# Optimization experiments

Measured on AMD Instinct MI355X. Metric: run time of the kernel, lower is better.

Reference implementation:

```python
import jax, jax.numpy as jnp
import numpy as np

T, N, DH, E = 4, 50000, 64, 800000
BN_EPS = 1e-5


def setup_inputs() -> dict:
    key = jax.random.key(0)
    ks = jax.random.split(key, 8)
    node_data = jax.random.normal(ks[0], (T, N, DH), dtype=jnp.float32)
    edge_weight = jax.random.uniform(ks[1], (E,), dtype=jnp.float32)
    W1 = jax.random.normal(ks[2], (DH, 3 * DH), dtype=jnp.float32) * 0.05
    b1 = jax.random.normal(ks[3], (DH,), dtype=jnp.float32) * 0.05
    gamma = jnp.ones((3 * DH,), dtype=jnp.float32)
    beta = jnp.zeros((3 * DH,), dtype=jnp.float32)
    src = jax.random.randint(ks[4], (E,), 0, N)
    dst = jax.random.randint(ks[5], (E,), 0, N)
    return {"node_data": node_data, "edge_weight": edge_weight, "W1": W1,
            "b1": b1, "gamma": gamma, "beta": beta, "src": src, "dst": dst}


def reference(node_data, edge_weight, W1, b1, gamma, beta, src, dst):
    # --- sparse weighted neighbor aggregation (torch.bmm with sparse ew) ---
    # msg[t, e, :] = w_e * x[t, src_e, :]
    msg = node_data[:, src, :] * edge_weight[None, :, None]          # [T, E, dh]
    agg = jnp.zeros((T, N, DH), jnp.float32).at[:, dst, :].add(msg)  # [T, N, dh]
    # Z = torch.sparse.sum(ew, dim=2); Z[Z==0]=1 (degree normalization)
    Z = jnp.zeros((N,), jnp.float32).at[dst].add(edge_weight)
    Z = jnp.where(Z == 0, 1.0, Z)
    avg_neighbor = agg / Z[None, :, None]
    # prev_state: zeros at t=0, shifted node_data otherwise
    prev = jnp.concatenate([jnp.zeros((1, N, DH), jnp.float32), node_data[:-1]], axis=0)
    inp = jnp.concatenate([node_data, prev, avg_neighbor], axis=2).reshape(T * N, 3 * DH)
    # --- ReluFCN with batchnorm (training-mode batch stats, biased var) ---
    mu = jnp.mean(inp, axis=0)
    var = jnp.mean(jnp.square(inp - mu), axis=0)
    xhat = (inp - mu) * jax.lax.rsqrt(var + BN_EPS) * gamma + beta
    out = jax.nn.relu(xhat @ W1.T + b1)
    return out.reshape(T, N, DH)
```

## Files before the change

### kernel.cpp

```cpp
#include <hip/hip_runtime.h>

#define TT 4
#define NN 50000
#define DH 64
#define EE 800000
#define BN_EPS 1e-5f
#define NB 196
#define G1 64
#define G2 256
#define EB 2048
#define AGG_B 2048
#define AGG_W (AGG_B*4)
#define MAIN_B 2048
#define FOLD_B 8

typedef __attribute__((ext_vector_type(8))) short short8;
typedef __attribute__((ext_vector_type(4))) float floatx4;

#define WS_DEG      0
#define WS_FLAGS    200704
#define WS_ROWSTART 201728
#define WS_PX       401920
#define WS_PX2      467456
#define WS_PA       532992
#define WS_PA2      598528
#define WS_W1EFF    664064
#define WS_B1EFF    688640
#define WS_PACKED   1048576
#define WS_XB       8388608
#define WS_AVGB     34078720
#define WS_RANK     34078720

__device__ __forceinline__ unsigned short f2b(float f) {
    unsigned int u = __float_as_uint(f);
    unsigned int r = (u + 0x7FFFu + ((u >> 16) & 1u)) >> 16;
    return (unsigned short)r;
}
__device__ __forceinline__ float b2f(unsigned short u) {
    return __uint_as_float((unsigned int)u << 16);
}

__global__ __launch_bounds__(256) void k_prep_stats(
    const float* __restrict__ x, unsigned short* __restrict__ xb,
    float* __restrict__ PX, float* __restrict__ PX2,
    int* __restrict__ deg, int* __restrict__ flags) {
    int t = blockIdx.y;
    int tid = threadIdx.x;
    int pb = t * G1 + blockIdx.x;
    int gid = pb * 256 + tid;
    if (gid < NN) deg[gid] = 0;
    else if (gid < NN + NB) flags[gid - NN] = 0;

    int g = blockIdx.x * 256 + tid;
    const floatx4* xt = (const floatx4*)(x + (size_t)t * NN * 64);
    float s[4] = {0.f, 0.f, 0.f, 0.f}, s2[4] = {0.f, 0.f, 0.f, 0.f};
    for (int v = g; v < NN * 16; v += G1 * 256) {
        floatx4 d = __builtin_nontemporal_load(&xt[v]);
        ushort4 o;
        o.x = f2b(d.x); o.y = f2b(d.y); o.z = f2b(d.z); o.w = f2b(d.w);
        *(ushort4*)(xb + (size_t)(v >> 4) * 256 + t * 64 + (v & 15) * 4) = o;
        s[0] += d.x; s2[0] += d.x * d.x;
        s[1] += d.y; s2[1] += d.y * d.y;
        s[2] += d.z; s2[2] += d.z * d.z;
        s[3] += d.w; s2[3] += d.w * d.w;
    }
    __shared__ float ls[256 * 4], ls2[256 * 4];
#pragma unroll
    for (int j = 0; j < 4; ++j) { ls[tid * 4 + j] = s[j]; ls2[tid * 4 + j] = s2[j]; }
    __syncthreads();
    if (tid < 64) {
        int g16 = tid >> 2, comp = tid & 3;
        float rs = 0.f, rs2 = 0.f;
#pragma unroll
        for (int k = 0; k < 16; ++k) {
            int j = g16 + 16 * k;
            rs += ls[j * 4 + comp]; rs2 += ls2[j * 4 + comp];
        }
        int slot = (t * G1 + blockIdx.x) * 64 + tid;
        PX[slot] = rs; PX2[slot] = rs2;
    }
}

__global__ __launch_bounds__(256) void k_rank(const int* __restrict__ dst,
                                              int* __restrict__ deg,
                                              int* __restrict__ rank) {
    for (int e = blockIdx.x * 256 + threadIdx.x; e < EE; e += EB * 256)
        rank[e] = atomicAdd(&deg[dst[e]], 1);
}

__global__ __launch_bounds__(256) void k_scan_lb(
    const int* __restrict__ deg, int* __restrict__ flags,
    int* __restrict__ row_start) {
    int b = blockIdx.x, tid = threadIdx.x;
    int i = b * 256 + tid;
    int v = (i < NN) ? deg[i] : 0;
    __shared__ int ls[256];
    ls[tid] = v;
    __syncthreads();
    for (int off = 1; off < 256; off <<= 1) {
        int t = (tid >= off) ? ls[tid - off] : 0;
        __syncthreads();
        ls[tid] += t;
        __syncthreads();
    }
    int incl = ls[tid];
    if (tid == 0) atomicExch(&flags[b], ls[255] + 1);
    __shared__ int pre_s;
    if (tid == 0) pre_s = 0;
    __syncthreads();
    if (tid < b) {
        int f;
        do { f = atomicAdd(&flags[tid], 0); } while (f == 0);
        atomicAdd(&pre_s, f - 1);
    }
    __syncthreads();
    int excl = pre_s + incl - v;
    if (i < NN) row_start[i] = excl;
    if (i == NN - 1) row_start[NN] = excl + v;
}

__global__ __launch_bounds__(256) void k_fill2(
    const int* __restrict__ src, const int* __restrict__ dst,
    const float* __restrict__ ew, const int* __restrict__ rank,
    const int* __restrict__ row_start, int2* __restrict__ packed) {
    for (int e = blockIdx.x * 256 + threadIdx.x; e < EE; e += EB * 256) {
        int p = row_start[dst[e]] + rank[e];
        packed[p] = make_int2(src[e], __float_as_int(ew[e]));
    }
}

__global__ __launch_bounds__(256) void k_agg(
    const unsigned short* __restrict__ xb, const int2* __restrict__ packed,
    const int* __restrict__ row_start, unsigned short* __restrict__ avgb) {
    int wv = __builtin_amdgcn_readfirstlane(threadIdx.x >> 6);
    int l = threadIdx.x & 63;
    int wgid = blockIdx.x * 4 + wv;
    const ushort4* xl = (const ushort4*)xb + l;
    for (int n = wgid; n < NN; n += AGG_W) {
        int rs = row_start[n], re = row_start[n + 1];
        float a0 = 0.f, a1 = 0.f, a2 = 0.f, a3 = 0.f, wsum = 0.f;
        for (int e = rs; e < re; e += 8) {
            int rem = re - e;
            int2 p[8];
#pragma unroll
            for (int j = 0; j < 8; ++j) p[j] = packed[e + j];
            ushort4 v[8];
#pragma unroll
            for (int j = 0; j < 8; ++j) {
                int sidx = (j < rem) ? p[j].x : 0;
                v[j] = xl[(size_t)sidx * 64];
            }
#pragma unroll
            for (int j = 0; j < 8; ++j) {
                float w = (j < rem) ? __int_as_float(p[j].y) : 0.f;
                wsum += w;
                a0 = fmaf(w, b2f(v[j].x), a0);
                a1 = fmaf(w, b2f(v[j].y), a1);
                a2 = fmaf(w, b2f(v[j].z), a2);
                a3 = fmaf(w, b2f(v[j].w), a3);
            }
        }
        float rz = (wsum == 0.f) ? 1.f : (1.f / wsum);
        ushort4 o;
        o.x = f2b(a0 * rz); o.y = f2b(a1 * rz);
        o.z = f2b(a2 * rz); o.w = f2b(a3 * rz);
        *((ushort4*)avgb + (size_t)n * 64 + l) = o;
    }
}

__global__ __launch_bounds__(256) void k_stats_avg(
    const unsigned short* __restrict__ avgb, float* __restrict__ PA,
    float* __restrict__ PA2) {
    int tid = threadIdx.x;
    int g = blockIdx.x * 256 + tid;
    const short8* av = (const short8*)avgb;
    float s[8], s2[8];
#pragma unroll
    for (int j = 0; j < 8; ++j) { s[j] = 0.f; s2[j] = 0.f; }
    for (int v = g; v < TT * NN * 8; v += G2 * 256) {
        short8 d = av[v];
#pragma unroll
        for (int j = 0; j < 8; ++j) {
            float f = b2f((unsigned short)d[j]);
            s[j] += f; s2[j] += f * f;
        }
    }
    __shared__ float ls[256 * 8], ls2[256 * 8];
#pragma unroll
    for (int j = 0; j < 8; ++j) { ls[tid * 8 + j] = s[j]; ls2[tid * 8 + j] = s2[j]; }
    __syncthreads();
    if (tid < 64) {
        int g8 = tid >> 3, comp = tid & 7;
        float rs = 0.f, rs2 = 0.f;
#pragma unroll
        for (int k = 0; k < 32; ++k) {
            int j = g8 + 8 * k;
            rs += ls[j * 8 + comp]; rs2 += ls2[j * 8 + comp];
        }
        PA[blockIdx.x * 64 + tid] = rs;
        PA2[blockIdx.x * 64 + tid] = rs2;
    }
}

__global__ void k_fold(const float* __restrict__ W1, const float* __restrict__ b1,
                       const float* __restrict__ gamma, const float* __restrict__ beta,
                       const float* __restrict__ PX, const float* __restrict__ PX2,
                       const float* __restrict__ PA, const float* __restrict__ PA2,
                       unsigned short* __restrict__ W1eff, float* __restrict__ b1eff) {
    __shared__ float gS[192], hS[192];
    int c = threadIdx.x;
    const float inv = 1.0f / (float)(TT * NN);
    if (c < 192) {
        float s = 0.f, s2 = 0.f;
        if (c < 64) {
            for (int i = 0; i < TT * G1; ++i) { s += PX[i * 64 + c]; s2 += PX2[i * 64 + c]; }
        } else if (c < 128) {
            int cc = c - 64;
            for (int i = 0; i < (TT - 1) * G1; ++i) { s += PX[i * 64 + cc]; s2 += PX2[i * 64 + cc]; }
        } else {
            int cc = c - 128;
            for (int i = 0; i < G2; ++i) { s += PA[i * 64 + cc]; s2 += PA2[i * 64 + cc]; }
        }
        float mu = s * inv, ex2 = s2 * inv;
        float var = ex2 - mu * mu;
        float g = gamma[c] / sqrtf(var + BN_EPS);
        gS[c] = g;
        hS[c] = beta[c] - mu * g;
    }
    __syncthreads();
    for (int i = blockIdx.x * 192 + c; i < 64 * 192; i += FOLD_B * 192)
        W1eff[i] = f2b(W1[i] * gS[c]);
    if (c < 8) {
        int o = blockIdx.x * 8 + c;
        float acc = b1[o];
        for (int cc = 0; cc < 192; ++cc) acc += hS[cc] * W1[o * 192 + cc];
        b1eff[o] = acc;
    }
}

__global__ __launch_bounds__(256) void k_main(
    const unsigned short* __restrict__ xb, const unsigned short* __restrict__ avgb,
    const unsigned short* __restrict__ Wb, const float* __restrict__ bias,
    float* __restrict__ out) {
    int wave = threadIdx.x >> 6;
    int lane = threadIdx.x & 63;
    int m = lane & 15;
    int q = lane >> 4;
    const short8 zf = (short8){0, 0, 0, 0, 0, 0, 0, 0};

    for (int tile = blockIdx.x; tile < (TT * NN) / 64; tile += MAIN_B) {
        int r0 = tile * 64 + wave * 16;
        int t = r0 / NN;
        int n0 = r0 - t * NN;

        size_t nb = (size_t)(n0 + m) * 256 + (size_t)t * 64 + q * 8;
        const unsigned short* xrow = xb + nb;
        const unsigned short* arow = avgb + nb;
        bool has_prev = (t >= 1);

        floatx4 acc[4];
#pragma unroll
        for (int ct = 0; ct < 4; ++ct) acc[ct] = (floatx4){0.f, 0.f, 0.f, 0.f};

#pragma unroll
        for (int kc = 0; kc < 6; ++kc) {
            short8 a;
            if (kc < 2) {
                a = *(const short8*)(xrow + kc * 32);
            } else if (kc < 4) {
                a = has_prev ? *(const short8*)(xrow - 64 + (kc - 2) * 32) : zf;
            } else {
                a = *(const short8*)(arow + (kc - 4) * 32);
            }
#pragma unroll
            for (int ct = 0; ct < 4; ++ct) {
                short8 b = *(const short8*)(Wb + (size_t)(ct * 16 + m) * 192 + kc * 32 + q * 8);
                acc[ct] = __builtin_amdgcn_mfma_f32_16x16x32_bf16(a, b, acc[ct], 0, 0, 0);
            }
        }

#pragma unroll
        for (int ct = 0; ct < 4; ++ct) {
            float bv = bias[ct * 16 + m];
#pragma unroll
            for (int i = 0; i < 4; ++i) {
                int row = q * 4 + i;
                __builtin_nontemporal_store(fmaxf(acc[ct][i] + bv, 0.f),
                                            &out[(size_t)(r0 + row) * 64 + ct * 16 + m]);
            }
        }
    }
}

extern "C" void kernel_launch(void* const* d_in, const int* in_sizes, int n_in,
                              void* d_out, int out_size, void* d_ws, size_t ws_size,
                              hipStream_t stream) {
    const float* x     = (const float*)d_in[0];
    const float* ew    = (const float*)d_in[1];
    const float* W1    = (const float*)d_in[2];
    const float* b1    = (const float*)d_in[3];
    const float* gamma = (const float*)d_in[4];
    const float* beta  = (const float*)d_in[5];
    const int*   src   = (const int*)d_in[6];
    const int*   dst   = (const int*)d_in[7];
    float* out = (float*)d_out;
    char*  ws  = (char*)d_ws;

    int*   deg      = (int*)(ws + WS_DEG);
    int*   flags    = (int*)(ws + WS_FLAGS);
    int*   row_start= (int*)(ws + WS_ROWSTART);
    float* PX       = (float*)(ws + WS_PX);
    float* PX2      = (float*)(ws + WS_PX2);
    float* PA       = (float*)(ws + WS_PA);
    float* PA2      = (float*)(ws + WS_PA2);
    unsigned short* W1eff = (unsigned short*)(ws + WS_W1EFF);
    float* b1eff    = (float*)(ws + WS_B1EFF);
    int2*  packed   = (int2*)(ws + WS_PACKED);
    unsigned short* xb   = (unsigned short*)(ws + WS_XB);
    unsigned short* avgb = (unsigned short*)(ws + WS_AVGB);
    int*   rank     = (int*)(ws + WS_RANK);

    k_prep_stats<<<dim3(G1, TT), 256, 0, stream>>>(x, xb, PX, PX2, deg, flags);

    k_rank<<<EB, 256, 0, stream>>>(dst, deg, rank);

    k_scan_lb<<<NB, 256, 0, stream>>>(deg, flags, row_start);

    k_fill2<<<EB, 256, 0, stream>>>(src, dst, ew, rank, row_start, packed);

    k_agg<<<AGG_B, 256, 0, stream>>>(xb, packed, row_start, avgb);

    k_stats_avg<<<G2, 256, 0, stream>>>(avgb, PA, PA2);

    k_fold<<<FOLD_B, 192, 0, stream>>>(W1, b1, gamma, beta, PX, PX2, PA, PA2, W1eff, b1eff);

    k_main<<<MAIN_B, 256, 0, stream>>>(xb, avgb, W1eff, b1eff, out);
}
```

Before: 316.1 us.

## Fuse CSR build into cooperative kernel with sharded degree counters; fuse avg stats into agg

Replaces the separate rank, scan and fill kernels with one cooperative kernel that keeps dst and rank in registers across grid syncs. Degree atomics are spread over 8 shards to cut contention. The per-column statistics of the averaged neighbours are now accumulated inside the aggregation kernel, which removes a second pass over avgb. The cost is four grid-wide barriers, a dependence on cooperative launch residency (1024 blocks), and a fold step that now reduces 2048 partial sums instead of 256.

```diff
diff --git a/kernel.cpp b/kernel.cpp
--- a/kernel.cpp
+++ b/kernel.cpp
@@ -1,14 +1,19 @@
 #include <hip/hip_runtime.h>
+#include <hip/hip_cooperative_groups.h>
+
+namespace cg = cooperative_groups;
 
 #define TT 4
 #define NN 50000
 #define DH 64
 #define EE 800000
 #define BN_EPS 1e-5f
-#define NB 196
 #define G1 64
-#define G2 256
-#define EB 2048
+#define NSH 8
+#define NBLD 1024
+#define BTH (NBLD*256)
+#define EPT 4
+#define NBSC 196
 #define AGG_B 2048
 #define AGG_W (AGG_B*4)
 #define MAIN_B 2048
@@ -18,18 +23,17 @@
 typedef __attribute__((ext_vector_type(4))) float floatx4;
 
 #define WS_DEG      0
-#define WS_FLAGS    200704
-#define WS_ROWSTART 201728
-#define WS_PX       401920
-#define WS_PX2      467456
-#define WS_PA       532992
-#define WS_PA2      598528
-#define WS_W1EFF    664064
-#define WS_B1EFF    688640
-#define WS_PACKED   1048576
-#define WS_XB       8388608
-#define WS_AVGB     34078720
-#define WS_RANK     34078720
+#define WS_PA       0
+#define WS_PA2      524288
+#define WS_PART     1600000
+#define WS_ROWSTART 1601024
+#define WS_PX       1801088
+#define WS_PX2      1866624
+#define WS_W1EFF    1932160
+#define WS_B1EFF    1956736
+#define WS_PACKED   1957376
+#define WS_XB       8357888
+#define WS_AVGB     33957888
 
 __device__ __forceinline__ unsigned short f2b(float f) {
     unsigned int u = __float_as_uint(f);
@@ -43,13 +47,11 @@
 __global__ __launch_bounds__(256) void k_prep_stats(
     const float* __restrict__ x, unsigned short* __restrict__ xb,
     float* __restrict__ PX, float* __restrict__ PX2,
-    int* __restrict__ deg, int* __restrict__ flags) {
+    int* __restrict__ deg) {
     int t = blockIdx.y;
     int tid = threadIdx.x;
-    int pb = t * G1 + blockIdx.x;
-    int gid = pb * 256 + tid;
-    if (gid < NN) deg[gid] = 0;
-    else if (gid < NN + NB) flags[gid - NN] = 0;
+    int zid = (t * G1 + blockIdx.x) * 256 + tid;
+    for (int i = zid; i < NSH * NN; i += 65536) deg[i] = 0;
 
     int g = blockIdx.x * 256 + tid;
     const floatx4* xt = (const floatx4*)(x + (size_t)t * NN * 64);
@@ -81,61 +83,99 @@
     }
 }
 
-__global__ __launch_bounds__(256) void k_rank(const int* __restrict__ dst,
-                                              int* __restrict__ deg,
-                                              int* __restrict__ rank) {
-    for (int e = blockIdx.x * 256 + threadIdx.x; e < EE; e += EB * 256)
-        rank[e] = atomicAdd(&deg[dst[e]], 1);
-}
-
-__global__ __launch_bounds__(256) void k_scan_lb(
-    const int* __restrict__ deg, int* __restrict__ flags,
-    int* __restrict__ row_start) {
-    int b = blockIdx.x, tid = threadIdx.x;
-    int i = b * 256 + tid;
-    int v = (i < NN) ? deg[i] : 0;
+__global__ __launch_bounds__(256, 4) void k_build(
+    const int* __restrict__ src, const int* __restrict__ dst,
+    const float* __restrict__ ew,
+    int* __restrict__ deg,
+    int* __restrict__ part,
+    int* __restrict__ row_start,
+    int2* __restrict__ packed) {
+    cg::grid_group grid = cg::this_grid();
+    int tid = threadIdx.x, bid = blockIdx.x;
+    int gtid = bid * 256 + tid;
+    int sh = bid & (NSH - 1);
+
+    int dstR[EPT], rnkR[EPT];
+#pragma unroll
+    for (int k = 0; k < EPT; ++k) {
+        int e = gtid + k * BTH;
+        if (e < EE) {
+            int d = dst[e];
+            dstR[k] = d;
+            rnkR[k] = atomicAdd(&deg[sh * NN + d], 1);
+        }
+    }
+    grid.sync();
+
     __shared__ int ls[256];
-    ls[tid] = v;
+    __shared__ int lsp[256];
+    int n = gtid;
+    int tot = 0;
+    if (n < NN) {
+        int run = 0;
+#pragma unroll
+        for (int s = 0; s < NSH; ++s) {
+            int c = deg[s * NN + n];
+            deg[s * NN + n] = run;
+            run += c;
+        }
+        tot = run;
+    }
+    ls[tid] = tot;
     __syncthreads();
     for (int off = 1; off < 256; off <<= 1) {
-        int t = (tid >= off) ? ls[tid - off] : 0;
+        int tv = (tid >= off) ? ls[tid - off] : 0;
         __syncthreads();
-        ls[tid] += t;
+        ls[tid] += tv;
         __syncthreads();
     }
     int incl = ls[tid];
-    if (tid == 0) atomicExch(&flags[b], ls[255] + 1);
-    __shared__ int pre_s;
-    if (tid == 0) pre_s = 0;
-    __syncthreads();
-    if (tid < b) {
-        int f;
-        do { f = atomicAdd(&flags[tid], 0); } while (f == 0);
-        atomicAdd(&pre_s, f - 1);
-    }
-    __syncthreads();
-    int excl = pre_s + incl - v;
-    if (i < NN) row_start[i] = excl;
-    if (i == NN - 1) row_start[NN] = excl + v;
-}
-
-__global__ __launch_bounds__(256) void k_fill2(
-    const int* __restrict__ src, const int* __restrict__ dst,
-    const float* __restrict__ ew, const int* __restrict__ rank,
-    const int* __restrict__ row_start, int2* __restrict__ packed) {
-    for (int e = blockIdx.x * 256 + threadIdx.x; e < EE; e += EB * 256) {
-        int p = row_start[dst[e]] + rank[e];
-        packed[p] = make_int2(src[e], __float_as_int(ew[e]));
+    if (tid == 255 && bid < NBSC) part[bid] = incl;
+    grid.sync();
+
+    if (bid == 0) {
+        int v = (tid < NBSC) ? part[tid] : 0;
+        lsp[tid] = v;
+        __syncthreads();
+        for (int off = 1; off < 256; off <<= 1) {
+            int tv = (tid >= off) ? lsp[tid - off] : 0;
+            __syncthreads();
+            lsp[tid] += tv;
+            __syncthreads();
+        }
+        if (tid < NBSC) part[tid] = lsp[tid] - v;
+    }
+    grid.sync();
+
+    if (n < NN) {
+        int excl = part[bid] + incl - tot;
+        row_start[n] = excl;
+        if (n == NN - 1) row_start[NN] = excl + tot;
+    }
+    grid.sync();
+
+#pragma unroll
+    for (int k = 0; k < EPT; ++k) {
+        int e = gtid + k * BTH;
+        if (e < EE) {
+            int d = dstR[k];
+            int p = row_start[d] + deg[sh * NN + d] + rnkR[k];
+            packed[p] = make_int2(src[e], __float_as_int(ew[e]));
+        }
     }
 }
 
 __global__ __launch_bounds__(256) void k_agg(
     const unsigned short* __restrict__ xb, const int2* __restrict__ packed,
-    const int* __restrict__ row_start, unsigned short* __restrict__ avgb) {
+    const int* __restrict__ row_start, unsigned short* __restrict__ avgb,
+    float* __restrict__ PA, float* __restrict__ PA2) {
     int wv = __builtin_amdgcn_readfirstlane(threadIdx.x >> 6);
-    int l = threadIdx.x & 63;
+    int tid = threadIdx.x;
+    int l = tid & 63;
     int wgid = blockIdx.x * 4 + wv;
     const ushort4* xl = (const ushort4*)xb + l;
+    float sA[4] = {0.f, 0.f, 0.f, 0.f}, sA2[4] = {0.f, 0.f, 0.f, 0.f};
+
     for (int n = wgid; n < NN; n += AGG_W) {
         int rs = row_start[n], re = row_start[n + 1];
         float a0 = 0.f, a1 = 0.f, a2 = 0.f, a3 = 0.f, wsum = 0.f;
@@ -165,37 +205,24 @@
         o.x = f2b(a0 * rz); o.y = f2b(a1 * rz);
         o.z = f2b(a2 * rz); o.w = f2b(a3 * rz);
         *((ushort4*)avgb + (size_t)n * 64 + l) = o;
-    }
-}
-
-__global__ __launch_bounds__(256) void k_stats_avg(
-    const unsigned short* __restrict__ avgb, float* __restrict__ PA,
-    float* __restrict__ PA2) {
-    int tid = threadIdx.x;
-    int g = blockIdx.x * 256 + tid;
-    const short8* av = (const short8*)avgb;
-    float s[8], s2[8];
-#pragma unroll
-    for (int j = 0; j < 8; ++j) { s[j] = 0.f; s2[j] = 0.f; }
-    for (int v = g; v < TT * NN * 8; v += G2 * 256) {
-        short8 d = av[v];
-#pragma unroll
-        for (int j = 0; j < 8; ++j) {
-            float f = b2f((unsigned short)d[j]);
-            s[j] += f; s2[j] += f * f;
-        }
-    }
-    __shared__ float ls[256 * 8], ls2[256 * 8];
-#pragma unroll
-    for (int j = 0; j < 8; ++j) { ls[tid * 8 + j] = s[j]; ls2[tid * 8 + j] = s2[j]; }
+        float f0 = b2f(o.x), f1 = b2f(o.y), f2v = b2f(o.z), f3 = b2f(o.w);
+        sA[0] += f0; sA2[0] += f0 * f0;
+        sA[1] += f1; sA2[1] += f1 * f1;
+        sA[2] += f2v; sA2[2] += f2v * f2v;
+        sA[3] += f3; sA2[3] += f3 * f3;
+    }
+
+    __shared__ float ls[256 * 4], ls2[256 * 4];
+#pragma unroll
+    for (int j = 0; j < 4; ++j) { ls[tid * 4 + j] = sA[j]; ls2[tid * 4 + j] = sA2[j]; }
     __syncthreads();
     if (tid < 64) {
-        int g8 = tid >> 3, comp = tid & 7;
+        int g15 = tid >> 2, j = tid & 3;
         float rs = 0.f, rs2 = 0.f;
 #pragma unroll
-        for (int k = 0; k < 32; ++k) {
-            int j = g8 + 8 * k;
-            rs += ls[j * 8 + comp]; rs2 += ls2[j * 8 + comp];
+        for (int k = 0; k < 16; ++k) {
+            int st = k * 16 + g15;
+            rs += ls[st * 4 + j]; rs2 += ls2[st * 4 + j];
         }
         PA[blockIdx.x * 64 + tid] = rs;
         PA2[blockIdx.x * 64 + tid] = rs2;
@@ -219,7 +246,7 @@
             for (int i = 0; i < (TT - 1) * G1; ++i) { s += PX[i * 64 + cc]; s2 += PX2[i * 64 + cc]; }
         } else {
             int cc = c - 128;
-            for (int i = 0; i < G2; ++i) { s += PA[i * 64 + cc]; s2 += PA2[i * 64 + cc]; }
+            for (int i = 0; i < AGG_B; ++i) { s += PA[i * 64 + cc]; s2 += PA2[i * 64 + cc]; }
         }
         float mu = s * inv, ex2 = s2 * inv;
         float var = ex2 - mu * mu;
@@ -307,7 +334,7 @@
     char*  ws  = (char*)d_ws;
 
     int*   deg      = (int*)(ws + WS_DEG);
-    int*   flags    = (int*)(ws + WS_FLAGS);
+    int*   part     = (int*)(ws + WS_PART);
     int*   row_start= (int*)(ws + WS_ROWSTART);
     float* PX       = (float*)(ws + WS_PX);
     float* PX2      = (float*)(ws + WS_PX2);
@@ -318,19 +345,17 @@
     int2*  packed   = (int2*)(ws + WS_PACKED);
     unsigned short* xb   = (unsigned short*)(ws + WS_XB);
     unsigned short* avgb = (unsigned short*)(ws + WS_AVGB);
-    int*   rank     = (int*)(ws + WS_RANK);
-
-    k_prep_stats<<<dim3(G1, TT), 256, 0, stream>>>(x, xb, PX, PX2, deg, flags);
-
-    k_rank<<<EB, 256, 0, stream>>>(dst, deg, rank);
-
-    k_scan_lb<<<NB, 256, 0, stream>>>(deg, flags, row_start);
-
-    k_fill2<<<EB, 256, 0, stream>>>(src, dst, ew, rank, row_start, packed);
-
-    k_agg<<<AGG_B, 256, 0, stream>>>(xb, packed, row_start, avgb);
-
-    k_stats_avg<<<G2, 256, 0, stream>>>(avgb, PA, PA2);
+
+    k_prep_stats<<<dim3(G1, TT), 256, 0, stream>>>(x, xb, PX, PX2, deg);
+
+    {
+        void* args[] = {(void*)&src, (void*)&dst, (void*)&ew, (void*)&deg,
+                        (void*)&part, (void*)&row_start, (void*)&packed};
+        hipLaunchCooperativeKernel((const void*)k_build, dim3(NBLD), dim3(256),
+                                   args, 0, stream);
+    }
+
+    k_agg<<<AGG_B, 256, 0, stream>>>(xb, packed, row_start, avgb, PA, PA2);
 
     k_fold<<<FOLD_B, 192, 0, stream>>>(W1, b1, gamma, beta, PX, PX2, PA, PA2, W1eff, b1eff);
 
```

Result: slower. 773.6 us (+144.7%).

## Fuse neighbor-average BN statistics into aggregation kernel and split aggregation launch

Applied to the files above, without the earlier changes.

Per-column sum and sum-of-squares statistics for the averaged neighbor features are now gathered inside the aggregation kernel, from the bf16-rounded outputs it already holds in registers. Each block reduces them and atomically adds into per-block partials, so the separate stats kernel and its full re-read of the averaged buffer are gone. The partial buffers are zeroed in the fill kernel, and the workspace is laid out again so they reuse the degree and flag area. Aggregation is also split into two launches over node halves, which adds a launch and atomics and makes the fold kernel reduce more partials.

```diff
diff --git a/kernel.cpp b/kernel.cpp
--- a/kernel.cpp
+++ b/kernel.cpp
@@ -7,29 +7,29 @@
 #define BN_EPS 1e-5f
 #define NB 196
 #define G1 64
-#define G2 256
 #define EB 2048
 #define AGG_B 2048
 #define AGG_W (AGG_B*4)
 #define MAIN_B 2048
 #define FOLD_B 8
+#define NHALF 25000
 
 typedef __attribute__((ext_vector_type(8))) short short8;
 typedef __attribute__((ext_vector_type(4))) float floatx4;
 
+#define WS_PA       0
+#define WS_PA2      524288
 #define WS_DEG      0
 #define WS_FLAGS    200704
-#define WS_ROWSTART 201728
-#define WS_PX       401920
-#define WS_PX2      467456
-#define WS_PA       532992
-#define WS_PA2      598528
-#define WS_W1EFF    664064
-#define WS_B1EFF    688640
-#define WS_PACKED   1048576
+#define WS_ROWSTART 1048576
+#define WS_PX       1249280
+#define WS_PX2      1314816
+#define WS_W1EFF    1380352
+#define WS_B1EFF    1404928
+#define WS_PACKED   1441792
 #define WS_XB       8388608
-#define WS_AVGB     34078720
-#define WS_RANK     34078720
+#define WS_AVGB     33988608
+#define WS_RANK     33988608
 
 __device__ __forceinline__ unsigned short f2b(float f) {
     unsigned int u = __float_as_uint(f);
@@ -122,8 +122,11 @@
 __global__ __launch_bounds__(256) void k_fill2(
     const int* __restrict__ src, const int* __restrict__ dst,
     const float* __restrict__ ew, const int* __restrict__ rank,
-    const int* __restrict__ row_start, int2* __restrict__ packed) {
-    for (int e = blockIdx.x * 256 + threadIdx.x; e < EE; e += EB * 256) {
+    const int* __restrict__ row_start, int2* __restrict__ packed,
+    float* __restrict__ PA) {
+    int gtid = blockIdx.x * 256 + threadIdx.x;
+    if (gtid < 2 * AGG_B * 64) PA[gtid] = 0.f;
+    for (int e = gtid; e < EE; e += EB * 256) {
         int p = row_start[dst[e]] + rank[e];
         packed[p] = make_int2(src[e], __float_as_int(ew[e]));
     }
@@ -131,12 +134,16 @@
 
 __global__ __launch_bounds__(256) void k_agg(
     const unsigned short* __restrict__ xb, const int2* __restrict__ packed,
-    const int* __restrict__ row_start, unsigned short* __restrict__ avgb) {
+    const int* __restrict__ row_start, unsigned short* __restrict__ avgb,
+    float* __restrict__ PA, float* __restrict__ PA2, int lo, int hi) {
     int wv = __builtin_amdgcn_readfirstlane(threadIdx.x >> 6);
-    int l = threadIdx.x & 63;
+    int tid = threadIdx.x;
+    int l = tid & 63;
     int wgid = blockIdx.x * 4 + wv;
     const ushort4* xl = (const ushort4*)xb + l;
-    for (int n = wgid; n < NN; n += AGG_W) {
+    float sA[4] = {0.f, 0.f, 0.f, 0.f}, sA2[4] = {0.f, 0.f, 0.f, 0.f};
+
+    for (int n = lo + wgid; n < hi; n += AGG_W) {
         int rs = row_start[n], re = row_start[n + 1];
         float a0 = 0.f, a1 = 0.f, a2 = 0.f, a3 = 0.f, wsum = 0.f;
         for (int e = rs; e < re; e += 8) {
@@ -165,40 +172,27 @@
         o.x = f2b(a0 * rz); o.y = f2b(a1 * rz);
         o.z = f2b(a2 * rz); o.w = f2b(a3 * rz);
         *((ushort4*)avgb + (size_t)n * 64 + l) = o;
-    }
-}
-
-__global__ __launch_bounds__(256) void k_stats_avg(
-    const unsigned short* __restrict__ avgb, float* __restrict__ PA,
-    float* __restrict__ PA2) {
-    int tid = threadIdx.x;
-    int g = blockIdx.x * 256 + tid;
-    const short8* av = (const short8*)avgb;
-    float s[8], s2[8];
-#pragma unroll
-    for (int j = 0; j < 8; ++j) { s[j] = 0.f; s2[j] = 0.f; }
-    for (int v = g; v < TT * NN * 8; v += G2 * 256) {
-        short8 d = av[v];
-#pragma unroll
-        for (int j = 0; j < 8; ++j) {
-            float f = b2f((unsigned short)d[j]);
-            s[j] += f; s2[j] += f * f;
-        }
-    }
-    __shared__ float ls[256 * 8], ls2[256 * 8];
-#pragma unroll
-    for (int j = 0; j < 8; ++j) { ls[tid * 8 + j] = s[j]; ls2[tid * 8 + j] = s2[j]; }
+        float f0 = b2f(o.x), f1 = b2f(o.y), f2v = b2f(o.z), f3 = b2f(o.w);
+        sA[0] += f0; sA2[0] += f0 * f0;
+        sA[1] += f1; sA2[1] += f1 * f1;
+        sA[2] += f2v; sA2[2] += f2v * f2v;
+        sA[3] += f3; sA2[3] += f3 * f3;
+    }
+
+    __shared__ float ls[256 * 4], ls2[256 * 4];
+#pragma unroll
+    for (int j = 0; j < 4; ++j) { ls[tid * 4 + j] = sA[j]; ls2[tid * 4 + j] = sA2[j]; }
     __syncthreads();
     if (tid < 64) {
-        int g8 = tid >> 3, comp = tid & 7;
+        int g15 = tid >> 2, j = tid & 3;
         float rs = 0.f, rs2 = 0.f;
 #pragma unroll
-        for (int k = 0; k < 32; ++k) {
-            int j = g8 + 8 * k;
-            rs += ls[j * 8 + comp]; rs2 += ls2[j * 8 + comp];
-        }
-        PA[blockIdx.x * 64 + tid] = rs;
-        PA2[blockIdx.x * 64 + tid] = rs2;
+        for (int k = 0; k < 16; ++k) {
+            int st = k * 16 + g15;
+            rs += ls[st * 4 + j]; rs2 += ls2[st * 4 + j];
+        }
+        atomicAdd(&PA[blockIdx.x * 64 + tid], rs);
+        atomicAdd(&PA2[blockIdx.x * 64 + tid], rs2);
     }
 }
 
@@ -219,7 +213,7 @@
             for (int i = 0; i < (TT - 1) * G1; ++i) { s += PX[i * 64 + cc]; s2 += PX2[i * 64 + cc]; }
         } else {
             int cc = c - 128;
-            for (int i = 0; i < G2; ++i) { s += PA[i * 64 + cc]; s2 += PA2[i * 64 + cc]; }
+            for (int i = 0; i < AGG_B; ++i) { s += PA[i * 64 + cc]; s2 += PA2[i * 64 + cc]; }
         }
         float mu = s * inv, ex2 = s2 * inv;
         float var = ex2 - mu * mu;
@@ -326,11 +320,10 @@
 
     k_scan_lb<<<NB, 256, 0, stream>>>(deg, flags, row_start);
 
-    k_fill2<<<EB, 256, 0, stream>>>(src, dst, ew, rank, row_start, packed);
-
-    k_agg<<<AGG_B, 256, 0, stream>>>(xb, packed, row_start, avgb);
-
-    k_stats_avg<<<G2, 256, 0, stream>>>(avgb, PA, PA2);
+    k_fill2<<<EB, 256, 0, stream>>>(src, dst, ew, rank, row_start, packed, PA);
+
+    k_agg<<<AGG_B, 256, 0, stream>>>(xb, packed, row_start, avgb, PA, PA2, 0, NHALF);
+    k_agg<<<AGG_B, 256, 0, stream>>>(xb, packed, row_start, avgb, PA, PA2, NHALF, NN);
 
     k_fold<<<FOLD_B, 192, 0, stream>>>(W1, b1, gamma, beta, PX, PX2, PA, PA2, W1eff, b1eff);
 
```

Result: slower. 373.1 us (+18.0%).
